# Kernel optimization log

Hardware: AMD Instinct MI355X
Metric: run time of the kernel (lower is better)

Reference implementation:

```python
import jax, jax.numpy as jnp
import numpy as np

B, S, HID = 2, 2048, 4096
H, KV, D = 32, 8, 128      # num_heads, num_kv_heads, head_dim
G = H // KV                 # num_key_value_groups
N = 16                      # num_neighbors
RH = HID // 4               # r_hidden_size (compression_factor=4)


def setup_inputs() -> dict:
    key = jax.random.key(0)
    ks = jax.random.split(key, 6)
    return {
        "hidden_states": jax.random.normal(ks[0], (B, S, HID), jnp.float32),
        "retrieved_hidden_states": jax.random.normal(ks[1], (B, S, N, RH), jnp.float32),
        # nn.Linear weights [out_features, in_features], std = in_features**-0.5
        "Wq": jax.random.normal(ks[2], (H * D, HID), jnp.float32) * HID ** -0.5,
        "Wk": jax.random.normal(ks[3], (KV * D, RH), jnp.float32) * RH ** -0.5,
        "Wv": jax.random.normal(ks[4], (KV * D, RH), jnp.float32) * RH ** -0.5,
        "Wo": jax.random.normal(ks[5], (HID, H * D), jnp.float32) * (H * D) ** -0.5,
    }


def reference(hidden_states, retrieved_hidden_states, Wq, Wk, Wv, Wo):
    b, s, hid = hidden_states.shape
    n = retrieved_hidden_states.shape[2]
    scaler = D ** -0.5
    # queries: [b,s,H*D] -> grouped [b,s,KV,G,D] (head h = kv_head*G + g, matching repeat_kv)
    q = (hidden_states @ Wq.T * scaler).reshape(b, s, KV, G, D)
    # keys/values: torch computes [b,s,n,KV*D] then flat-views as [b,s,KV,n,D]; replicate exactly
    k = (retrieved_hidden_states @ Wk.T).reshape(b, s, KV, n, D)
    v = (retrieved_hidden_states @ Wv.T).reshape(b, s, KV, n, D)
    # per-query attention over n neighbors; grouped einsum avoids materializing repeat_kv expand
    scores = jnp.einsum('bskgd,bsknd->bskgn', q, k)   # [b,s,KV,G,n]
    attn = jax.nn.softmax(scores, axis=-1)
    out = jnp.einsum('bskgn,bsknd->bskgd', attn, v).reshape(b, s, H * D)
    return out @ Wo.T
```

## Files before the change

### kernel.cpp

```cpp
#include <hip/hip_runtime.h>
#include <hip/hip_bf16.h>
#include <stdint.h>

#define DEV_INLINE __device__ __forceinline__

typedef __attribute__((ext_vector_type(4))) float f32x4;
typedef __attribute__((ext_vector_type(8))) __bf16 bf16x8;
typedef __attribute__((ext_vector_type(8))) unsigned short u16x8;

constexpr int Hh = 32, KVc = 8, Dd = 128, Gg = 4, Nn = 16;

DEV_INLINE unsigned short f32_to_bf16(float f) {
  unsigned u = __float_as_uint(f);
  u += 0x7fffu + ((u >> 16) & 1u);
  return (unsigned short)(u >> 16);
}
DEV_INLINE float bf16_lo(unsigned u) { return __uint_as_float(u << 16); }
DEV_INLINE float bf16_hi(unsigned u) { return __uint_as_float(u & 0xffff0000u); }

__global__ void cast_f32_bf16_kernel(const float* __restrict__ src,
                                     unsigned short* __restrict__ dst,
                                     int n4, float scale) {
  int i = blockIdx.x * blockDim.x + threadIdx.x;
  int stride = gridDim.x * blockDim.x;
  const f32x4* s4 = reinterpret_cast<const f32x4*>(src);
  ushort4* d4 = reinterpret_cast<ushort4*>(dst);
  for (; i < n4; i += stride) {
    f32x4 v = s4[i];
    ushort4 o;
    o.x = f32_to_bf16(v.x * scale);
    o.y = f32_to_bf16(v.y * scale);
    o.z = f32_to_bf16(v.z * scale);
    o.w = f32_to_bf16(v.w * scale);
    d4[i] = o;
  }
}

template <bool OUT_BF16>
__global__ __launch_bounds__(512) void gemm256_kernel(
    const unsigned short* __restrict__ A,
    const unsigned short* __restrict__ Bw,
    void* __restrict__ Cout,
    int M, int N, int K) {
  __shared__ alignas(16) unsigned short Als[4][256 * 32];
  __shared__ alignas(16) unsigned short Bls[4][256 * 32];
  const int tid = threadIdx.x;
  const int wave = tid >> 6, lane = tid & 63;
  const int wm = wave >> 2, wn = wave & 3;
  const int lrow = lane & 15, lhi = lane >> 4;
  const int swslot = (lhi ^ ((lrow >> 1) & 3)) << 4;

  const int ntn = N >> 8;
  const int nwg = gridDim.x, bid = blockIdx.x;
  const int swz = ((nwg & 7) == 0) ? ((bid & 7) * (nwg >> 3) + (bid >> 3)) : bid;
  const int tm = swz / ntn, tn = swz - tm * ntn;

  const unsigned short* Abase = A + (long)tm * 256 * K;
  const unsigned short* Bbase = Bw + (long)tn * 256 * K;
  const int ktiles = K >> 5;

  auto stage = [&](const unsigned short* gbase, unsigned short* lslot, int k0) {
#pragma unroll
    for (int j = 0; j < 2; ++j) {
      int c = (j << 9) + tid;
      int row = c >> 2;
      int gslot = (c & 3) ^ ((row >> 1) & 3);
      const unsigned short* g = gbase + (long)row * K + k0 + (gslot << 3);
      int ldsoff = (((j << 9) + (wave << 6)) << 4);
      __builtin_amdgcn_global_load_lds(
          (const __attribute__((address_space(1))) unsigned int*)g,
          (__attribute__((address_space(3))) unsigned int*)((char*)lslot + ldsoff),
          16, 0, 0);
    }
  };

  f32x4 acc[8][4];
#pragma unroll
  for (int m = 0; m < 8; ++m)
#pragma unroll
    for (int n = 0; n < 4; ++n) acc[m][n] = {0.f, 0.f, 0.f, 0.f};

#pragma unroll
  for (int p = 0; p < 3; ++p) {
    if (p < ktiles) {
      stage(Abase, Als[p], p << 5);
      stage(Bbase, Bls[p], p << 5);
    }
  }
  if (ktiles > 2) asm volatile("s_waitcnt vmcnt(8)" ::: "memory");
  else            asm volatile("s_waitcnt vmcnt(0)" ::: "memory");
  __builtin_amdgcn_s_barrier();

  bf16x8 afr[4], bfr[4];
  for (int t = 0; t < ktiles; ++t) {
    const int slot = t & 3, ps = (t + 3) & 3;
    const char* Ac = (const char*)Als[slot];
    const char* Bc = (const char*)Bls[slot];

#pragma unroll
    for (int n = 0; n < 4; ++n)
      bfr[n] = *reinterpret_cast<const bf16x8*>(
          Bc + (((wn << 6) + (n << 4) + lrow) << 6) + swslot);
#pragma unroll
    for (int m = 0; m < 4; ++m)
      afr[m] = *reinterpret_cast<const bf16x8*>(
          Ac + (((wm << 7) + (m << 4) + lrow) << 6) + swslot);
    if (t + 3 < ktiles) stage(Abase, Als[ps], (t + 3) << 5);
    __builtin_amdgcn_s_barrier();
    asm volatile("s_waitcnt lgkmcnt(0)");
    __builtin_amdgcn_s_setprio(1);
#pragma unroll
    for (int m = 0; m < 4; ++m)
#pragma unroll
      for (int n = 0; n < 4; ++n)
        acc[m][n] = __builtin_amdgcn_mfma_f32_16x16x32_bf16(afr[m], bfr[n],
                                                            acc[m][n], 0, 0, 0);
    __builtin_amdgcn_s_setprio(0);
    __builtin_amdgcn_s_barrier();

#pragma unroll
    for (int m = 0; m < 4; ++m)
      afr[m] = *reinterpret_cast<const bf16x8*>(
          Ac + (((wm << 7) + 64 + (m << 4) + lrow) << 6) + swslot);
    if (t + 3 < ktiles) stage(Bbase, Bls[ps], (t + 3) << 5);
    __builtin_amdgcn_s_barrier();
    asm volatile("s_waitcnt lgkmcnt(0)");
    __builtin_amdgcn_s_setprio(1);
#pragma unroll
    for (int m = 0; m < 4; ++m)
#pragma unroll
      for (int n = 0; n < 4; ++n)
        acc[m + 4][n] = __builtin_amdgcn_mfma_f32_16x16x32_bf16(
            afr[m], bfr[n], acc[m + 4][n], 0, 0, 0);
    __builtin_amdgcn_s_setprio(0);
    if (t + 3 < ktiles)      asm volatile("s_waitcnt vmcnt(8)" ::: "memory");
    else if (t + 2 < ktiles) asm volatile("s_waitcnt vmcnt(4)" ::: "memory");
    else if (t + 1 < ktiles) asm volatile("s_waitcnt vmcnt(0)" ::: "memory");
    __builtin_amdgcn_s_barrier();
  }

#pragma unroll
  for (int m = 0; m < 8; ++m) {
#pragma unroll
    for (int n = 0; n < 4; ++n) {
      long r0 = (long)tm * 256 + (wm << 7) + (m << 4) + (lhi << 2);
      long c0 = (long)tn * 256 + (wn << 6) + (n << 4) + lrow;
#pragma unroll
      for (int r = 0; r < 4; ++r) {
        float v = acc[m][n][r];
        if constexpr (OUT_BF16)
          ((unsigned short*)Cout)[(r0 + r) * N + c0] = f32_to_bf16(v);
        else
          ((float*)Cout)[(r0 + r) * N + c0] = v;
      }
    }
  }
}

__global__ __launch_bounds__(256) void attn_kernel(
    const unsigned short* __restrict__ Q,
    const unsigned short* __restrict__ Kf,
    const unsigned short* __restrict__ Vf,
    unsigned short* __restrict__ O) {
  const int tid = threadIdx.x;
  const int wave = tid >> 6;
  const int lane = tid & 63;
  const int sl = blockIdx.x * 4 + wave;
  const int bs = sl >> 3;
  const int kv = sl & 7;
  const int g = lane >> 4;
  const int i = lane & 15;

  const unsigned short* qrow = Q + (long)bs * (Hh * Dd) + (kv * Gg + g) * Dd;
  const int ni = 2 * kv + (i >> 3);
  const unsigned short* krow =
      Kf + ((long)bs * Nn + ni) * (KVc * Dd) + (i & 7) * Dd;

  float s = 0.f;
#pragma unroll
  for (int c = 0; c < 16; ++c) {
    uint4 qu = *reinterpret_cast<const uint4*>(qrow + c * 8);
    uint4 ku = *reinterpret_cast<const uint4*>(krow + c * 8);
    s += bf16_lo(qu.x) * bf16_lo(ku.x) + bf16_hi(qu.x) * bf16_hi(ku.x);
    s += bf16_lo(qu.y) * bf16_lo(ku.y) + bf16_hi(qu.y) * bf16_hi(ku.y);
    s += bf16_lo(qu.z) * bf16_lo(ku.z) + bf16_hi(qu.z) * bf16_hi(ku.z);
    s += bf16_lo(qu.w) * bf16_lo(ku.w) + bf16_hi(qu.w) * bf16_hi(ku.w);
  }

  float mx = s;
#pragma unroll
  for (int off = 8; off >= 1; off >>= 1) mx = fmaxf(mx, __shfl_xor(mx, off));
  float p = __expf(s - mx);
  float sum = p;
#pragma unroll
  for (int off = 8; off >= 1; off >>= 1) sum += __shfl_xor(sum, off);
  p = p / sum;

  float o[8] = {0.f, 0.f, 0.f, 0.f, 0.f, 0.f, 0.f, 0.f};
  const long vbase = (long)bs * Nn * (KVc * Dd);
#pragma unroll
  for (int ii = 0; ii < 16; ++ii) {
    float pi = __shfl(p, (lane & 48) | ii);
    const unsigned short* vrow = Vf + vbase +
        (long)(2 * kv + (ii >> 3)) * (KVc * Dd) + (ii & 7) * Dd + i * 8;
    uint4 vu = *reinterpret_cast<const uint4*>(vrow);
    o[0] += pi * bf16_lo(vu.x); o[1] += pi * bf16_hi(vu.x);
    o[2] += pi * bf16_lo(vu.y); o[3] += pi * bf16_hi(vu.y);
    o[4] += pi * bf16_lo(vu.z); o[5] += pi * bf16_hi(vu.z);
    o[6] += pi * bf16_lo(vu.w); o[7] += pi * bf16_hi(vu.w);
  }
  u16x8 ov;
#pragma unroll
  for (int d = 0; d < 8; ++d) ov[d] = f32_to_bf16(o[d]);
  *reinterpret_cast<u16x8*>(O + (long)bs * (Hh * Dd) + (kv * Gg + g) * Dd +
                            i * 8) = ov;
}

extern "C" void kernel_launch(void* const* d_in, const int* in_sizes, int n_in,
                              void* d_out, int out_size, void* d_ws,
                              size_t ws_size, hipStream_t stream) {
  (void)in_sizes; (void)n_in; (void)out_size; (void)ws_size;
  const float* hs = (const float*)d_in[0];
  const float* rhs = (const float*)d_in[1];
  const float* Wq = (const float*)d_in[2];
  const float* Wk = (const float*)d_in[3];
  const float* Wv = (const float*)d_in[4];
  const float* Wo = (const float*)d_in[5];
  float* out = (float*)d_out;

  char* ws = (char*)d_ws;
  size_t off = 0;
  auto alloc = [&](size_t bytes) { char* p = ws + off; off += bytes; return p; };
  unsigned short* hsb  = (unsigned short*)alloc(16777216ull * 2);
  unsigned short* Wqb  = (unsigned short*)alloc(16777216ull * 2);
  unsigned short* rhsb = (unsigned short*)alloc(67108864ull * 2);
  unsigned short* Wkb  = (unsigned short*)alloc(1048576ull * 2);
  unsigned short* Wvb  = (unsigned short*)alloc(1048576ull * 2);
  unsigned short* Wob  = (unsigned short*)alloc(16777216ull * 2);
  unsigned short* Qb   = (unsigned short*)alloc(16777216ull * 2);
  unsigned short* Kb   = (unsigned short*)alloc(67108864ull * 2);
  unsigned short* Vb   = (unsigned short*)alloc(67108864ull * 2);
  unsigned short* Ab   = (unsigned short*)alloc(16777216ull * 2);

  const float scaler = 0.08838834764831845f;

  cast_f32_bf16_kernel<<<2048, 256, 0, stream>>>(hs, hsb, 16777216 / 4, 1.f);
  cast_f32_bf16_kernel<<<2048, 256, 0, stream>>>(Wq, Wqb, 16777216 / 4, scaler);
  cast_f32_bf16_kernel<<<4096, 256, 0, stream>>>(rhs, rhsb, 67108864 / 4, 1.f);
  cast_f32_bf16_kernel<<<512, 256, 0, stream>>>(Wk, Wkb, 1048576 / 4, 1.f);
  cast_f32_bf16_kernel<<<512, 256, 0, stream>>>(Wv, Wvb, 1048576 / 4, 1.f);
  cast_f32_bf16_kernel<<<2048, 256, 0, stream>>>(Wo, Wob, 16777216 / 4, 1.f);

  gemm256_kernel<true><<<256, 512, 0, stream>>>(hsb, Wqb, Qb, 4096, 4096, 4096);
  gemm256_kernel<true><<<1024, 512, 0, stream>>>(rhsb, Wkb, Kb, 65536, 1024, 1024);
  gemm256_kernel<true><<<1024, 512, 0, stream>>>(rhsb, Wvb, Vb, 65536, 1024, 1024);
  attn_kernel<<<8192, 256, 0, stream>>>(Qb, Kb, Vb, Ab);
  gemm256_kernel<false><<<256, 512, 0, stream>>>(Ab, Wob, out, 4096, 4096, 4096);
}
```

Measured before the change: 864.4 us.

## Software-pipeline LDS fragment reads across MFMA halves in bf16 GEMM

```diff
diff --git a/kernel.cpp b/kernel.cpp
--- a/kernel.cpp
+++ b/kernel.cpp
@@ -37,7 +37,7 @@
 }
 
 template <bool OUT_BF16>
-__global__ __launch_bounds__(512) void gemm256_kernel(
+__global__ __launch_bounds__(512, 2) void gemm256_kernel(
     const unsigned short* __restrict__ A,
     const unsigned short* __restrict__ Bw,
     void* __restrict__ Cout,
@@ -74,6 +74,20 @@
     }
   };
 
+#define RD_B(dst, Bc)                                                      \
+  _Pragma("unroll") for (int n = 0; n < 4; ++n) dst[n] =                   \
+      *reinterpret_cast<const bf16x8*>(                                    \
+          (Bc) + (((wn << 6) + (n << 4) + lrow) << 6) + swslot);
+#define RD_A(dst, Ac, mh)                                                  \
+  _Pragma("unroll") for (int m = 0; m < 4; ++m) dst[m] =                   \
+      *reinterpret_cast<const bf16x8*>(                                    \
+          (Ac) + (((wm << 7) + ((mh) << 6) + (m << 4) + lrow) << 6) + swslot);
+#define MFMA16(accrow, af, bf)                                             \
+  _Pragma("unroll") for (int m = 0; m < 4; ++m)                            \
+  _Pragma("unroll") for (int n = 0; n < 4; ++n)                            \
+      acc[(accrow) + m][n] = __builtin_amdgcn_mfma_f32_16x16x32_bf16(      \
+          af[m], bf[n], acc[(accrow) + m][n], 0, 0, 0);
+
   f32x4 acc[8][4];
 #pragma unroll
   for (int m = 0; m < 8; ++m)
@@ -91,51 +105,61 @@
   else            asm volatile("s_waitcnt vmcnt(0)" ::: "memory");
   __builtin_amdgcn_s_barrier();
 
-  bf16x8 afr[4], bfr[4];
-  for (int t = 0; t < ktiles; ++t) {
-    const int slot = t & 3, ps = (t + 3) & 3;
-    const char* Ac = (const char*)Als[slot];
-    const char* Bc = (const char*)Bls[slot];
-
-#pragma unroll
-    for (int n = 0; n < 4; ++n)
-      bfr[n] = *reinterpret_cast<const bf16x8*>(
-          Bc + (((wn << 6) + (n << 4) + lrow) << 6) + swslot);
-#pragma unroll
-    for (int m = 0; m < 4; ++m)
-      afr[m] = *reinterpret_cast<const bf16x8*>(
-          Ac + (((wm << 7) + (m << 4) + lrow) << 6) + swslot);
-    if (t + 3 < ktiles) stage(Abase, Als[ps], (t + 3) << 5);
-    __builtin_amdgcn_s_barrier();
-    asm volatile("s_waitcnt lgkmcnt(0)");
-    __builtin_amdgcn_s_setprio(1);
-#pragma unroll
-    for (int m = 0; m < 4; ++m)
-#pragma unroll
-      for (int n = 0; n < 4; ++n)
-        acc[m][n] = __builtin_amdgcn_mfma_f32_16x16x32_bf16(afr[m], bfr[n],
-                                                            acc[m][n], 0, 0, 0);
-    __builtin_amdgcn_s_setprio(0);
-    __builtin_amdgcn_s_barrier();
-
-#pragma unroll
-    for (int m = 0; m < 4; ++m)
-      afr[m] = *reinterpret_cast<const bf16x8*>(
-          Ac + (((wm << 7) + 64 + (m << 4) + lrow) << 6) + swslot);
-    if (t + 3 < ktiles) stage(Bbase, Bls[ps], (t + 3) << 5);
-    __builtin_amdgcn_s_barrier();
-    asm volatile("s_waitcnt lgkmcnt(0)");
-    __builtin_amdgcn_s_setprio(1);
-#pragma unroll
-    for (int m = 0; m < 4; ++m)
-#pragma unroll
-      for (int n = 0; n < 4; ++n)
-        acc[m + 4][n] = __builtin_amdgcn_mfma_f32_16x16x32_bf16(
-            afr[m], bfr[n], acc[m + 4][n], 0, 0, 0);
-    __builtin_amdgcn_s_setprio(0);
-    if (t + 3 < ktiles)      asm volatile("s_waitcnt vmcnt(8)" ::: "memory");
-    else if (t + 2 < ktiles) asm volatile("s_waitcnt vmcnt(4)" ::: "memory");
-    else if (t + 1 < ktiles) asm volatile("s_waitcnt vmcnt(0)" ::: "memory");
+  bf16x8 bfrE[4], afrE[4], bfrO[4], afrO[4], afrH[4];
+  RD_B(bfrE, (const char*)Bls[0]);
+  RD_A(afrE, (const char*)Als[0], 0);
+
+  for (int t0 = 0; t0 < ktiles; t0 += 2) {
+    const int t1 = t0 + 1;
+    const char* Ac0 = (const char*)Als[t0 & 3];
+    const char* Bc0 = (const char*)Bls[t0 & 3];
+    const char* Ac1 = (const char*)Als[t1 & 3];
+    const char* Bc1 = (const char*)Bls[t1 & 3];
+    const int sp = (t0 + 3) & 3;
+
+    RD_A(afrH, Ac0, 1);
+    if (t0 + 3 < ktiles) stage(Abase, Als[sp], (t0 + 3) << 5);
+    asm volatile("s_waitcnt lgkmcnt(4)" ::: "memory");
+    __builtin_amdgcn_s_setprio(1);
+    MFMA16(0, afrE, bfrE);
+    __builtin_amdgcn_s_setprio(0);
+    if (t0 + 3 < ktiles)      asm volatile("s_waitcnt vmcnt(6)" ::: "memory");
+    else if (t0 + 2 < ktiles) asm volatile("s_waitcnt vmcnt(4)" ::: "memory");
+    else                      asm volatile("s_waitcnt vmcnt(0)" ::: "memory");
+    __builtin_amdgcn_s_barrier();
+
+    RD_B(bfrO, Bc1);
+    RD_A(afrO, Ac1, 0);
+    if (t0 + 3 < ktiles) stage(Bbase, Bls[sp], (t0 + 3) << 5);
+    asm volatile("s_waitcnt lgkmcnt(8)" ::: "memory");
+    __builtin_amdgcn_s_setprio(1);
+    MFMA16(4, afrH, bfrE);
+    __builtin_amdgcn_s_setprio(0);
+    __builtin_amdgcn_s_barrier();
+
+    RD_A(afrH, Ac1, 1);
+    if (t1 + 3 < ktiles) stage(Abase, Als[t0 & 3], (t1 + 3) << 5);
+    asm volatile("s_waitcnt lgkmcnt(4)" ::: "memory");
+    __builtin_amdgcn_s_setprio(1);
+    MFMA16(0, afrO, bfrO);
+    __builtin_amdgcn_s_setprio(0);
+    if (t1 + 3 < ktiles)      asm volatile("s_waitcnt vmcnt(6)" ::: "memory");
+    else if (t1 + 2 < ktiles) asm volatile("s_waitcnt vmcnt(4)" ::: "memory");
+    else                      asm volatile("s_waitcnt vmcnt(0)" ::: "memory");
+    __builtin_amdgcn_s_barrier();
+
+    if (t0 + 2 < ktiles) {
+      const char* Bc2 = (const char*)Bls[(t0 + 2) & 3];
+      const char* Ac2 = (const char*)Als[(t0 + 2) & 3];
+      RD_B(bfrE, Bc2);
+      RD_A(afrE, Ac2, 0);
+    }
+    if (t1 + 3 < ktiles) stage(Bbase, Bls[t0 & 3], (t1 + 3) << 5);
+    if (t0 + 2 < ktiles) asm volatile("s_waitcnt lgkmcnt(8)" ::: "memory");
+    else                 asm volatile("s_waitcnt lgkmcnt(0)" ::: "memory");
+    __builtin_amdgcn_s_setprio(1);
+    MFMA16(4, afrH, bfrO);
+    __builtin_amdgcn_s_setprio(0);
     __builtin_amdgcn_s_barrier();
   }
 
@@ -155,6 +179,9 @@
       }
     }
   }
+#undef RD_A
+#undef RD_B
+#undef MFMA16
 }
 
 __global__ __launch_bounds__(256) void attn_kernel(
```

New measurement: 829.2 us. 4.1% less time.

## Switch GEMM to 32x32x16 MFMA with new LDS layout and merged staging

Applied to the files above, without the earlier changes.

```diff
diff --git a/kernel.cpp b/kernel.cpp
--- a/kernel.cpp
+++ b/kernel.cpp
@@ -5,6 +5,7 @@
 #define DEV_INLINE __device__ __forceinline__
 
 typedef __attribute__((ext_vector_type(4))) float f32x4;
+typedef __attribute__((ext_vector_type(16))) float f32x16;
 typedef __attribute__((ext_vector_type(8))) __bf16 bf16x8;
 typedef __attribute__((ext_vector_type(8))) unsigned short u16x8;
 
@@ -42,13 +43,15 @@
     const unsigned short* __restrict__ Bw,
     void* __restrict__ Cout,
     int M, int N, int K) {
-  __shared__ alignas(16) unsigned short Als[4][256 * 32];
-  __shared__ alignas(16) unsigned short Bls[4][256 * 32];
+  __shared__ alignas(16) unsigned short Als[4][8192];
+  __shared__ alignas(16) unsigned short Bls[4][8192];
   const int tid = threadIdx.x;
   const int wave = tid >> 6, lane = tid & 63;
   const int wm = wave >> 2, wn = wave & 3;
-  const int lrow = lane & 15, lhi = lane >> 4;
-  const int swslot = (lhi ^ ((lrow >> 1) & 3)) << 4;
+  const int baseA = wm * 8192 + ((lane >> 3) & 3) * 512 + (lane >> 5) * 128 +
+                    (lane & 7) * 16;
+  const int baseB = wn * 4096 + ((lane >> 3) & 3) * 512 + (lane >> 5) * 128 +
+                    (lane & 7) * 16;
 
   const int ntn = N >> 8;
   const int nwg = gridDim.x, bid = blockIdx.x;
@@ -63,9 +66,9 @@
 #pragma unroll
     for (int j = 0; j < 2; ++j) {
       int c = (j << 9) + tid;
-      int row = c >> 2;
-      int gslot = (c & 3) ^ ((row >> 1) & 3);
-      const unsigned short* g = gbase + (long)row * K + k0 + (gslot << 3);
+      int row = ((c >> 5) << 3) + (c & 7);
+      int kp = ((c >> 3) & 3) << 3;
+      const unsigned short* g = gbase + (long)row * K + k0 + kp;
       int ldsoff = (((j << 9) + (wave << 6)) << 4);
       __builtin_amdgcn_global_load_lds(
           (const __attribute__((address_space(1))) unsigned int*)g,
@@ -74,11 +77,13 @@
     }
   };
 
-  f32x4 acc[8][4];
-#pragma unroll
-  for (int m = 0; m < 8; ++m)
-#pragma unroll
-    for (int n = 0; n < 4; ++n) acc[m][n] = {0.f, 0.f, 0.f, 0.f};
+  f32x16 acc[4][2];
+#pragma unroll
+  for (int m = 0; m < 4; ++m)
+#pragma unroll
+    for (int n = 0; n < 2; ++n)
+#pragma unroll
+      for (int r = 0; r < 16; ++r) acc[m][n][r] = 0.f;
 
 #pragma unroll
   for (int p = 0; p < 3; ++p) {
@@ -91,67 +96,67 @@
   else            asm volatile("s_waitcnt vmcnt(0)" ::: "memory");
   __builtin_amdgcn_s_barrier();
 
-  bf16x8 afr[4], bfr[4];
   for (int t = 0; t < ktiles; ++t) {
-    const int slot = t & 3, ps = (t + 3) & 3;
-    const char* Ac = (const char*)Als[slot];
-    const char* Bc = (const char*)Bls[slot];
-
-#pragma unroll
-    for (int n = 0; n < 4; ++n)
-      bfr[n] = *reinterpret_cast<const bf16x8*>(
-          Bc + (((wn << 6) + (n << 4) + lrow) << 6) + swslot);
-#pragma unroll
-    for (int m = 0; m < 4; ++m)
-      afr[m] = *reinterpret_cast<const bf16x8*>(
-          Ac + (((wm << 7) + (m << 4) + lrow) << 6) + swslot);
-    if (t + 3 < ktiles) stage(Abase, Als[ps], (t + 3) << 5);
-    __builtin_amdgcn_s_barrier();
-    asm volatile("s_waitcnt lgkmcnt(0)");
+    const char* Ac = (const char*)Als[t & 3];
+    const char* Bc = (const char*)Bls[t & 3];
+    bf16x8 a0[4], a1[4], b0[2], b1[2];
+#pragma unroll
+    for (int m = 0; m < 4; ++m)
+      a0[m] = *reinterpret_cast<const bf16x8*>(Ac + baseA + m * 2048);
+#pragma unroll
+    for (int n = 0; n < 2; ++n)
+      b0[n] = *reinterpret_cast<const bf16x8*>(Bc + baseB + n * 2048);
+#pragma unroll
+    for (int m = 0; m < 4; ++m)
+      a1[m] = *reinterpret_cast<const bf16x8*>(Ac + baseA + m * 2048 + 256);
+#pragma unroll
+    for (int n = 0; n < 2; ++n)
+      b1[n] = *reinterpret_cast<const bf16x8*>(Bc + baseB + n * 2048 + 256);
+
+    if (t + 3 < ktiles) {
+      stage(Abase, Als[(t + 3) & 3], (t + 3) << 5);
+      stage(Bbase, Bls[(t + 3) & 3], (t + 3) << 5);
+    }
+
+    asm volatile("s_waitcnt lgkmcnt(6)" ::: "memory");
     __builtin_amdgcn_s_setprio(1);
 #pragma unroll
     for (int m = 0; m < 4; ++m)
 #pragma unroll
-      for (int n = 0; n < 4; ++n)
-        acc[m][n] = __builtin_amdgcn_mfma_f32_16x16x32_bf16(afr[m], bfr[n],
+      for (int n = 0; n < 2; ++n)
+        acc[m][n] = __builtin_amdgcn_mfma_f32_32x32x16_bf16(a0[m], b0[n],
+                                                            acc[m][n], 0, 0, 0);
+    asm volatile("s_waitcnt lgkmcnt(0)" ::: "memory");
+#pragma unroll
+    for (int m = 0; m < 4; ++m)
+#pragma unroll
+      for (int n = 0; n < 2; ++n)
+        acc[m][n] = __builtin_amdgcn_mfma_f32_32x32x16_bf16(a1[m], b1[n],
                                                             acc[m][n], 0, 0, 0);
     __builtin_amdgcn_s_setprio(0);
-    __builtin_amdgcn_s_barrier();
-
-#pragma unroll
-    for (int m = 0; m < 4; ++m)
-      afr[m] = *reinterpret_cast<const bf16x8*>(
-          Ac + (((wm << 7) + 64 + (m << 4) + lrow) << 6) + swslot);
-    if (t + 3 < ktiles) stage(Bbase, Bls[ps], (t + 3) << 5);
-    __builtin_amdgcn_s_barrier();
-    asm volatile("s_waitcnt lgkmcnt(0)");
-    __builtin_amdgcn_s_setprio(1);
-#pragma unroll
-    for (int m = 0; m < 4; ++m)
-#pragma unroll
-      for (int n = 0; n < 4; ++n)
-        acc[m + 4][n] = __builtin_amdgcn_mfma_f32_16x16x32_bf16(
-            afr[m], bfr[n], acc[m + 4][n], 0, 0, 0);
-    __builtin_amdgcn_s_setprio(0);
+
     if (t + 3 < ktiles)      asm volatile("s_waitcnt vmcnt(8)" ::: "memory");
     else if (t + 2 < ktiles) asm volatile("s_waitcnt vmcnt(4)" ::: "memory");
     else if (t + 1 < ktiles) asm volatile("s_waitcnt vmcnt(0)" ::: "memory");
     __builtin_amdgcn_s_barrier();
   }
 
-#pragma unroll
-  for (int m = 0; m < 8; ++m) {
-#pragma unroll
-    for (int n = 0; n < 4; ++n) {
-      long r0 = (long)tm * 256 + (wm << 7) + (m << 4) + (lhi << 2);
-      long c0 = (long)tn * 256 + (wn << 6) + (n << 4) + lrow;
-#pragma unroll
-      for (int r = 0; r < 4; ++r) {
+  const int cl = lane & 31;
+  const int rh = (lane >> 5) << 2;
+#pragma unroll
+  for (int m = 0; m < 4; ++m) {
+#pragma unroll
+    for (int n = 0; n < 2; ++n) {
+      long c0 = (long)tn * 256 + (wn << 6) + (n << 5) + cl;
+      long rb = (long)tm * 256 + (wm << 7) + (m << 5) + rh;
+#pragma unroll
+      for (int r = 0; r < 16; ++r) {
+        long row = rb + (r & 3) + ((r >> 2) << 3);
         float v = acc[m][n][r];
         if constexpr (OUT_BF16)
-          ((unsigned short*)Cout)[(r0 + r) * N + c0] = f32_to_bf16(v);
+          ((unsigned short*)Cout)[row * N + c0] = f32_to_bf16(v);
         else
-          ((float*)Cout)[(r0 + r) * N + c0] = v;
+          ((float*)Cout)[row * N + c0] = v;
       }
     }
   }
```

Result: no change. 861.3 us (-0.4%).

## Restructure GEMM to 64-wide K tiles with half-tile quadrant pipeline

Applied to the files above, without the earlier changes.

```diff
diff --git a/kernel.cpp b/kernel.cpp
--- a/kernel.cpp
+++ b/kernel.cpp
@@ -42,34 +42,41 @@
     const unsigned short* __restrict__ Bw,
     void* __restrict__ Cout,
     int M, int N, int K) {
-  __shared__ alignas(16) unsigned short Als[4][256 * 32];
-  __shared__ alignas(16) unsigned short Bls[4][256 * 32];
+  __shared__ alignas(16) unsigned short Als[2][2][8192];
+  __shared__ alignas(16) unsigned short Bls[2][2][8192];
   const int tid = threadIdx.x;
   const int wave = tid >> 6, lane = tid & 63;
   const int wm = wave >> 2, wn = wave & 3;
-  const int lrow = lane & 15, lhi = lane >> 4;
-  const int swslot = (lhi ^ ((lrow >> 1) & 3)) << 4;
+  const int r15 = lane & 15, lh = lane >> 4;
+  const int psl0 = (lh ^ (r15 & 7)) << 4;
+  const int psl1 = ((4 + lh) ^ (r15 & 7)) << 4;
+  const int aoff = (wm * 16 + r15) << 7;
+  const int boff = (wn * 16 + r15) << 7;
 
   const int ntn = N >> 8;
   const int nwg = gridDim.x, bid = blockIdx.x;
-  const int swz = ((nwg & 7) == 0) ? ((bid & 7) * (nwg >> 3) + (bid >> 3)) : bid;
+  const int swz = (bid & 7) * (nwg >> 3) + (bid >> 3);
   const int tm = swz / ntn, tn = swz - tm * ntn;
 
   const unsigned short* Abase = A + (long)tm * 256 * K;
   const unsigned short* Bbase = Bw + (long)tn * 256 * K;
-  const int ktiles = K >> 5;
-
-  auto stage = [&](const unsigned short* gbase, unsigned short* lslot, int k0) {
+  const int ktiles = K >> 6;
+  const int iters = ktiles >> 1;
+
+  auto stageh = [&](const unsigned short* gbase, unsigned short* lhalf, int t,
+                    int h) {
 #pragma unroll
     for (int j = 0; j < 2; ++j) {
       int c = (j << 9) + tid;
-      int row = c >> 2;
-      int gslot = (c & 3) ^ ((row >> 1) & 3);
-      const unsigned short* g = gbase + (long)row * K + k0 + (gslot << 3);
-      int ldsoff = (((j << 9) + (wave << 6)) << 4);
+      int row = c >> 3;
+      int sl = (c & 7) ^ (row & 7);
+      const unsigned short* g =
+          gbase + (long)((h << 7) + row) * K + (t << 6) + (sl << 3);
+      int ldsoff = ((j << 9) + (wave << 6)) << 4;
       __builtin_amdgcn_global_load_lds(
           (const __attribute__((address_space(1))) unsigned int*)g,
-          (__attribute__((address_space(3))) unsigned int*)((char*)lslot + ldsoff),
+          (__attribute__((address_space(3))) unsigned int*)((char*)lhalf +
+                                                            ldsoff),
           16, 0, 0);
     }
   };
@@ -80,71 +87,74 @@
 #pragma unroll
     for (int n = 0; n < 4; ++n) acc[m][n] = {0.f, 0.f, 0.f, 0.f};
 
-#pragma unroll
-  for (int p = 0; p < 3; ++p) {
-    if (p < ktiles) {
-      stage(Abase, Als[p], p << 5);
-      stage(Bbase, Bls[p], p << 5);
+  stageh(Abase, Als[0][0], 0, 0);
+  stageh(Bbase, Bls[0][0], 0, 0);
+  stageh(Bbase, Bls[0][1], 0, 1);
+  stageh(Abase, Als[0][1], 0, 1);
+  stageh(Abase, Als[1][0], 1, 0);
+  stageh(Bbase, Bls[1][0], 1, 0);
+  asm volatile("s_waitcnt vmcnt(4)" ::: "memory");
+  __builtin_amdgcn_s_barrier();
+
+  for (int i = 0; i < iters; ++i) {
+    const bool last = (i == iters - 1);
+#pragma unroll
+    for (int ti = 0; ti < 2; ++ti) {
+      const int t = 2 * i + ti;
+#pragma unroll
+      for (int q = 0; q < 4; ++q) {
+        const int mh = q >> 1, nh = q & 1;
+        const char* Ac = (const char*)Als[t & 1][mh];
+        const char* Bc = (const char*)Bls[t & 1][nh];
+        bf16x8 af[4][2], bf[2][2];
+#pragma unroll
+        for (int m = 0; m < 4; ++m) {
+          af[m][0] = *reinterpret_cast<const bf16x8*>(Ac + aoff + m * 4096 + psl0);
+          af[m][1] = *reinterpret_cast<const bf16x8*>(Ac + aoff + m * 4096 + psl1);
+        }
+#pragma unroll
+        for (int n = 0; n < 2; ++n) {
+          bf[n][0] = *reinterpret_cast<const bf16x8*>(Bc + boff + n * 8192 + psl0);
+          bf[n][1] = *reinterpret_cast<const bf16x8*>(Bc + boff + n * 8192 + psl1);
+        }
+        {
+          const int g = (t << 2) + q;
+          const int hh = g + 6, th = hh >> 2, hj = hh & 3;
+          if (th < ktiles) {
+            if (hj == 0)      stageh(Abase, Als[th & 1][0], th, 0);
+            else if (hj == 1) stageh(Bbase, Bls[th & 1][0], th, 0);
+            else if (hj == 2) stageh(Bbase, Bls[th & 1][1], th, 1);
+            else              stageh(Abase, Als[th & 1][1], th, 1);
+          }
+        }
+        __builtin_amdgcn_s_barrier();
+        asm volatile("s_waitcnt lgkmcnt(0)" ::: "memory");
+        __builtin_amdgcn_sched_barrier(0);
+        __builtin_amdgcn_s_setprio(1);
+#pragma unroll
+        for (int m = 0; m < 4; ++m)
+#pragma unroll
+          for (int n = 0; n < 2; ++n) {
+            acc[mh * 4 + m][nh * 2 + n] = __builtin_amdgcn_mfma_f32_16x16x32_bf16(
+                af[m][0], bf[n][0], acc[mh * 4 + m][nh * 2 + n], 0, 0, 0);
+            acc[mh * 4 + m][nh * 2 + n] = __builtin_amdgcn_mfma_f32_16x16x32_bf16(
+                af[m][1], bf[n][1], acc[mh * 4 + m][nh * 2 + n], 0, 0, 0);
+          }
+        __builtin_amdgcn_s_setprio(0);
+        __builtin_amdgcn_sched_barrier(0);
+        if (last) asm volatile("s_waitcnt vmcnt(0)" ::: "memory");
+        else      asm volatile("s_waitcnt vmcnt(6)" ::: "memory");
+        __builtin_amdgcn_s_barrier();
+      }
     }
   }
-  if (ktiles > 2) asm volatile("s_waitcnt vmcnt(8)" ::: "memory");
-  else            asm volatile("s_waitcnt vmcnt(0)" ::: "memory");
-  __builtin_amdgcn_s_barrier();
-
-  bf16x8 afr[4], bfr[4];
-  for (int t = 0; t < ktiles; ++t) {
-    const int slot = t & 3, ps = (t + 3) & 3;
-    const char* Ac = (const char*)Als[slot];
-    const char* Bc = (const char*)Bls[slot];
-
-#pragma unroll
-    for (int n = 0; n < 4; ++n)
-      bfr[n] = *reinterpret_cast<const bf16x8*>(
-          Bc + (((wn << 6) + (n << 4) + lrow) << 6) + swslot);
-#pragma unroll
-    for (int m = 0; m < 4; ++m)
-      afr[m] = *reinterpret_cast<const bf16x8*>(
-          Ac + (((wm << 7) + (m << 4) + lrow) << 6) + swslot);
-    if (t + 3 < ktiles) stage(Abase, Als[ps], (t + 3) << 5);
-    __builtin_amdgcn_s_barrier();
-    asm volatile("s_waitcnt lgkmcnt(0)");
-    __builtin_amdgcn_s_setprio(1);
-#pragma unroll
-    for (int m = 0; m < 4; ++m)
-#pragma unroll
-      for (int n = 0; n < 4; ++n)
-        acc[m][n] = __builtin_amdgcn_mfma_f32_16x16x32_bf16(afr[m], bfr[n],
-                                                            acc[m][n], 0, 0, 0);
-    __builtin_amdgcn_s_setprio(0);
-    __builtin_amdgcn_s_barrier();
-
-#pragma unroll
-    for (int m = 0; m < 4; ++m)
-      afr[m] = *reinterpret_cast<const bf16x8*>(
-          Ac + (((wm << 7) + 64 + (m << 4) + lrow) << 6) + swslot);
-    if (t + 3 < ktiles) stage(Bbase, Bls[ps], (t + 3) << 5);
-    __builtin_amdgcn_s_barrier();
-    asm volatile("s_waitcnt lgkmcnt(0)");
-    __builtin_amdgcn_s_setprio(1);
-#pragma unroll
-    for (int m = 0; m < 4; ++m)
-#pragma unroll
-      for (int n = 0; n < 4; ++n)
-        acc[m + 4][n] = __builtin_amdgcn_mfma_f32_16x16x32_bf16(
-            afr[m], bfr[n], acc[m + 4][n], 0, 0, 0);
-    __builtin_amdgcn_s_setprio(0);
-    if (t + 3 < ktiles)      asm volatile("s_waitcnt vmcnt(8)" ::: "memory");
-    else if (t + 2 < ktiles) asm volatile("s_waitcnt vmcnt(4)" ::: "memory");
-    else if (t + 1 < ktiles) asm volatile("s_waitcnt vmcnt(0)" ::: "memory");
-    __builtin_amdgcn_s_barrier();
-  }
 
 #pragma unroll
   for (int m = 0; m < 8; ++m) {
 #pragma unroll
     for (int n = 0; n < 4; ++n) {
-      long r0 = (long)tm * 256 + (wm << 7) + (m << 4) + (lhi << 2);
-      long c0 = (long)tn * 256 + (wn << 6) + (n << 4) + lrow;
+      long r0 = (long)tm * 256 + m * 32 + wm * 16 + lh * 4;
+      long c0 = (long)tn * 256 + n * 64 + wn * 16 + r15;
 #pragma unroll
       for (int r = 0; r < 4; ++r) {
         float v = acc[m][n][r];
```

After: 907.7 us. 1.05x slower.
